# Performance work log

Hardware: AMD Instinct MI355X
Metric: run time of the kernel (lower is better)

Reference implementation:

```python
import jax, jax.numpy as jnp
import numpy as np

B, S, D = 2, 2048, 1024
H, HD = 16, 64          # n_heads, head_dim
FF, HID = 4096, 8192    # d_ff, swiglu hidden (= 2*d_ff)


def _ln(x, eps=1e-5):
    # non-parametric LayerNorm (fp8_layernorm_noparam in source)
    m = jnp.mean(x, axis=-1, keepdims=True)
    v = jnp.var(x, axis=-1, keepdims=True)
    return (x - m) * jax.lax.rsqrt(v + eps)


def setup_inputs() -> dict:
    key = jax.random.key(0)
    ks = jax.random.split(key, 7)
    s = 0.02  # init std
    return {
        "x": jax.random.normal(ks[0], (B, S, D), jnp.float32),
        "Wq": jax.random.normal(ks[1], (D, D), jnp.float32) * s,
        "Wk": jax.random.normal(ks[2], (D, D), jnp.float32) * s,
        "Wv": jax.random.normal(ks[3], (D, D), jnp.float32) * s,
        "Wo": jax.random.normal(ks[4], (D, D), jnp.float32) * s,
        "Wff": jax.random.normal(ks[5], (HID, D), jnp.float32) * s,
        "Wout": jax.random.normal(ks[6], (FF, D), jnp.float32).T * s,  # [D, FF] -> stored as Linear weight [D_out=D, D_in=FF]
    }


def reference(x, Wq, Wk, Wv, Wo, Wff, Wout):
    b, s, d = x.shape
    # attention sub-block
    h = _ln(x)
    q = (h @ Wq.T).reshape(b, s, H, HD).transpose(0, 2, 1, 3)  # [B,H,S,HD]
    k = (h @ Wk.T).reshape(b, s, H, HD).transpose(0, 2, 1, 3)
    v = (h @ Wv.T).reshape(b, s, H, HD).transpose(0, 2, 1, 3)
    scale = 1.0 / float(HD) ** 0.5
    scores = jnp.einsum('bhqd,bhkd->bhqk', q, k) * scale        # [B,H,S,S] naive full matrix
    causal = jnp.tril(jnp.ones((s, s), dtype=bool))
    scores = jnp.where(causal, scores, jnp.finfo(scores.dtype).min)
    attn = jax.nn.softmax(scores, axis=-1)
    att = jnp.einsum('bhqk,bhkd->bhqd', attn, v)                # [B,H,S,HD]
    att = att.transpose(0, 2, 1, 3).reshape(b, s, d)
    x = x + att @ Wo.T
    # MLP sub-block (SwiGLU, OLMo Llama-style)
    h2 = _ln(x)
    ff = h2 @ Wff.T                                             # [B,S,HID]
    x1, x2 = jnp.split(ff, 2, axis=-1)
    g = jax.nn.silu(x1) * x2                                    # [B,S,FF]
    return x + g @ Wout.T
```

## Files before the change

### kernel.cpp

```cpp
#include <hip/hip_runtime.h>
#include <hip/hip_bf16.h>

#define B_ 2
#define S_ 2048
#define D_ 1024
#define H_ 16
#define FF_ 4096
#define M_ (B_*S_)

using u16 = unsigned short;
using u32 = unsigned int;
typedef __attribute__((ext_vector_type(8))) short short8;
typedef __attribute__((ext_vector_type(4))) float f32x4;
typedef __attribute__((ext_vector_type(16))) float f32x16;
typedef __attribute__((ext_vector_type(4))) unsigned short u16x4;
typedef __attribute__((ext_vector_type(4))) unsigned int u32x4;

static __device__ __forceinline__ u16 f2bf(float f) {
  __hip_bfloat16 h = __float2bfloat16(f);
  return *reinterpret_cast<u16*>(&h);
}
static __device__ __forceinline__ float bf2f(u16 u) {
  __hip_bfloat16 h; *reinterpret_cast<u16*>(&h) = u;
  return __bfloat162float(h);
}

#define GLDS(gp, lp) __builtin_amdgcn_global_load_lds( \
    (const __attribute__((address_space(1))) void*)(gp), \
    (__attribute__((address_space(3))) void*)(lp), 16, 0, 0)

#define MFMA16(a, b, c) __builtin_amdgcn_mfma_f32_16x16x32_bf16(a, b, c, 0, 0, 0)
#define VMC(n) asm volatile("s_waitcnt vmcnt(" #n ")" ::: "memory")
#define BAR() __builtin_amdgcn_s_barrier()

__global__ __launch_bounds__(256) void conv_f32_bf16(
    const float* __restrict__ src, u16* __restrict__ dst, int n4) {
  int i = blockIdx.x * 256 + threadIdx.x;
  if (i < n4) {
    float4 v = reinterpret_cast<const float4*>(src)[i];
    u16x4 o;
    o.x = f2bf(v.x); o.y = f2bf(v.y); o.z = f2bf(v.z); o.w = f2bf(v.w);
    reinterpret_cast<u16x4*>(dst)[i] = o;
  }
}

__global__ __launch_bounds__(256) void ln_rows(
    const float* __restrict__ x, u16* __restrict__ out) {
  int row = blockIdx.x;
  int t = threadIdx.x;
  float4 v = reinterpret_cast<const float4*>(x + (size_t)row * D_)[t];
  float s  = v.x + v.y + v.z + v.w;
  float ss = v.x*v.x + v.y*v.y + v.z*v.z + v.w*v.w;
  #pragma unroll
  for (int off = 1; off < 64; off <<= 1) {
    s  += __shfl_xor(s,  off, 64);
    ss += __shfl_xor(ss, off, 64);
  }
  __shared__ float rs[4], rss[4];
  int wid = t >> 6;
  if ((t & 63) == 0) { rs[wid] = s; rss[wid] = ss; }
  __syncthreads();
  s  = rs[0] + rs[1] + rs[2] + rs[3];
  ss = rss[0] + rss[1] + rss[2] + rss[3];
  float mean = s * (1.0f / D_);
  float var  = ss * (1.0f / D_) - mean * mean;
  float r = rsqrtf(var + 1e-5f);
  u16x4 o;
  o.x = f2bf((v.x - mean) * r);
  o.y = f2bf((v.y - mean) * r);
  o.z = f2bf((v.z - mean) * r);
  o.w = f2bf((v.w - mean) * r);
  reinterpret_cast<u16x4*>(out + (size_t)row * D_)[t] = o;
}

template<int MODE>
__global__ __launch_bounds__(256, 2) void gemm_bt2(
    const u16* __restrict__ A, const u16* __restrict__ W,
    void* __restrict__ C, const u16* __restrict__ aux,
    const float* __restrict__ res, int M, int N, int K)
{
  __shared__ u16 lds[32768];
  const int tid = threadIdx.x;
  const int wid = tid >> 6, lane = tid & 63;
  const int g = lane >> 4, c = lane & 15;
  const int gridN = N >> 7;
  int nwg = gridDim.x;
  int lin = blockIdx.x;
  lin = (lin & 7) * (nwg >> 3) + (lin >> 3);
  const int bm = lin / gridN, bn = lin % gridN;
  const int wm = wid >> 1, wn = wid & 1;
  const int NT = K >> 6;

  f32x4 acc[4][4];
  #pragma unroll
  for (int i = 0; i < 4; i++)
    #pragma unroll
    for (int j = 0; j < 4; j++) acc[i][j] = {0.f, 0.f, 0.f, 0.f};

  auto stage = [&](int sel, int t) {
    const u16* src = sel ? W : A;
    const int tilerow = (sel ? bn : bm) * 128;
    char* dst = (char*)&lds[sel * 16384 + (t & 1) * 8192];
    #pragma unroll
    for (int i = 0; i < 4; i++) {
      int j = i * 256 + tid;
      int row = j >> 3, col16 = j & 7;
      const u16* gp = src + (size_t)(tilerow + row) * K + t * 64 + ((col16 ^ (row & 7)) << 3);
      GLDS(gp, dst + j * 16);
    }
  };

  stage(0, 0); stage(1, 0);
  __syncthreads();

  for (int t = 0; t < NT; t++) {
    const int buf = t & 1;
    if (t + 1 < NT) { stage(0, t + 1); stage(1, t + 1); }

    short8 af[2][4], bfr[2][4];
    #pragma unroll
    for (int ks = 0; ks < 2; ks++)
      #pragma unroll
      for (int m = 0; m < 4; m++) {
        int rh = wm * 64 + m * 16 + c;
        af[ks][m] = *reinterpret_cast<const short8*>(
            &lds[buf * 8192 + rh * 64 + ((((ks << 2) | g) ^ (rh & 7)) << 3)]);
      }
    #pragma unroll
    for (int ks = 0; ks < 2; ks++)
      #pragma unroll
      for (int n = 0; n < 4; n++) {
        int rh = wn * 64 + n * 16 + c;
        bfr[ks][n] = *reinterpret_cast<const short8*>(
            &lds[16384 + buf * 8192 + rh * 64 + ((((ks << 2) | g) ^ (rh & 7)) << 3)]);
      }
    __builtin_amdgcn_s_setprio(1);
    #pragma unroll
    for (int m = 0; m < 4; m++)
      #pragma unroll
      for (int n = 0; n < 4; n++) {
        acc[m][n] = MFMA16(af[0][m], bfr[0][n], acc[m][n]);
        acc[m][n] = MFMA16(af[1][m], bfr[1][n], acc[m][n]);
      }
    __builtin_amdgcn_s_setprio(0);
    __syncthreads();
  }

  #pragma unroll
  for (int m = 0; m < 4; m++)
    #pragma unroll
    for (int n = 0; n < 4; n++)
      #pragma unroll
      for (int r = 0; r < 4; r++) {
        int gr = bm * 128 + wm * 64 + m * 16 + g * 4 + r;
        int gc = bn * 128 + wn * 64 + n * 16 + c;
        size_t idx = (size_t)gr * N + gc;
        float v = acc[m][n][r];
        if (MODE == 0) {
          ((u16*)C)[idx] = f2bf(v);
        } else if (MODE == 1) {
          ((float*)C)[idx] = v + res[idx];
        } else if (MODE == 2) {
          ((u16*)C)[idx] = f2bf(v / (1.0f + __expf(-v)));
        } else {
          ((u16*)C)[idx] = f2bf(v * bf2f(aux[idx]));
        }
      }
}

__global__ __launch_bounds__(256) void transpose_v(
    const u16* __restrict__ qkv, u16* __restrict__ vT) {
  __shared__ u16 t[64][66];
  int bh = blockIdx.y;
  int s0 = blockIdx.x * 64;
  int b = bh >> 4, h = bh & 15;
  int tid = threadIdx.x;
  #pragma unroll
  for (int it = 0; it < 2; it++) {
    int idx = it * 256 + tid;
    int row = idx >> 3;
    int cc  = (idx & 7) * 8;
    const u16* src = qkv + ((size_t)(b * S_ + s0 + row)) * 3072 + 2048 + h * 64 + cc;
    short8 v = *reinterpret_cast<const short8*>(src);
    #pragma unroll
    for (int j = 0; j < 8; j++) t[row][cc + j] = (u16)v[j];
  }
  __syncthreads();
  #pragma unroll
  for (int it = 0; it < 2; it++) {
    int idx = it * 256 + tid;
    int d  = idx >> 3;
    int sc = (idx & 7) * 8;
    short8 o;
    #pragma unroll
    for (int j = 0; j < 8; j++) o[j] = (short)t[sc + j][d];
    *reinterpret_cast<short8*>(vT + ((size_t)bh * 64 + d) * S_ + s0 + sc) = o;
  }
}

__global__ __launch_bounds__(256) void attn_split(
    const u16* __restrict__ qkv, const u16* __restrict__ vT,
    u16* __restrict__ pO, float* __restrict__ pML) {
  __shared__ u16 Kl[2][2048];
  __shared__ u16 Vl[2][2048];
  const int tid  = threadIdx.x;
  const int lane = tid & 63;
  const int wid  = tid >> 6;
  const int l31  = lane & 31;
  const int half = lane >> 5;

  int lin = blockIdx.x;
  int swz = (lin & 7) * 160 + (lin >> 3);
  int bh  = swz / 40;
  int j   = swz - bh * 40;
  int qq = 15, rem = j;
  while (rem > (qq >> 2)) { rem -= (qq >> 2) + 1; qq--; }
  int ci = rem;
  const int qt  = qq * 4 + wid;
  const int kt0 = ci * 16;
  const int nt  = min(qq * 4 + 3, kt0 + 15) - kt0;
  int ubase = (qt < 16) ? qt : (qt < 32) ? 16 + (qt - 16) * 2 + ci
            : (qt < 48) ? 48 + (qt - 32) * 3 + ci : 96 + (qt - 48) * 4 + ci;
  const int punit = bh * 160 + ubase;

  const int b = bh >> 4, hd = bh & 15;
  const int q_base = qt * 32;

  const u16* Qb = qkv + ((size_t)(b * S_ + q_base + l31)) * 3072 + hd * 64;
  const u16* Kb = qkv + (size_t)b * S_ * 3072 + 1024 + hd * 64;
  const u16* Vt = vT + (size_t)bh * 64 * S_;

  short8 qf[4];
  #pragma unroll
  for (int dt = 0; dt < 4; dt++) {
    short8 v = *reinterpret_cast<const short8*>(Qb + dt * 16 + half * 8);
    #pragma unroll
    for (int jj = 0; jj < 8; jj++) v[jj] = (short)f2bf(bf2f((u16)v[jj]) * 0.125f);
    qf[dt] = v;
  }

  auto stageKV = [&](int kt, int buf) {
    {
      int row = tid >> 3, cs = tid & 7;
      int c = cs ^ (row & 7);
      const u16* gp = Kb + (size_t)(kt * 32 + row) * 3072 + c * 8;
      GLDS(gp, (char*)&Kl[buf][0] + tid * 16);
    }
    {
      int row = tid >> 2, cs = tid & 3;
      int c = cs ^ (row & 3);
      const u16* gp = Vt + (size_t)row * S_ + kt * 32 + c * 8;
      GLDS(gp, (char*)&Vl[buf][0] + tid * 16);
    }
  };

  f32x16 o0, o1;
  #pragma unroll
  for (int r = 0; r < 16; r++) { o0[r] = 0.f; o1[r] = 0.f; }
  float m = -1e30f, lsum = 0.f;

  stageKV(kt0, 0);
  VMC(0); BAR();

  for (int i = 0; ; i++) {
    const int kt = kt0 + i;
    const int buf = i & 1;
    if (i < nt) stageKV(kt + 1, buf ^ 1);

    if (kt <= qt) {
      const bool diag = (kt == qt);
      short8 kfr[4], vfr[4];
      #pragma unroll
      for (int dt = 0; dt < 4; dt++) {
        int cs = (dt * 2 + half) ^ (l31 & 7);
        kfr[dt] = *reinterpret_cast<const short8*>((const char*)&Kl[buf][0] + l31 * 128 + cs * 16);
      }
      {
        int r0 = l31, r1 = 32 + l31;
        vfr[0] = *reinterpret_cast<const short8*>((const char*)&Vl[buf][0] + r0 * 64 + ((half       ^ (r0 & 3)) * 16));
        vfr[1] = *reinterpret_cast<const short8*>((const char*)&Vl[buf][0] + r0 * 64 + (((2 + half) ^ (r0 & 3)) * 16));
        vfr[2] = *reinterpret_cast<const short8*>((const char*)&Vl[buf][0] + r1 * 64 + ((half       ^ (r1 & 3)) * 16));
        vfr[3] = *reinterpret_cast<const short8*>((const char*)&Vl[buf][0] + r1 * 64 + (((2 + half) ^ (r1 & 3)) * 16));
      }

      f32x16 s;
      #pragma unroll
      for (int r = 0; r < 16; r++) s[r] = 0.f;
      __builtin_amdgcn_s_setprio(1);
      #pragma unroll
      for (int dt = 0; dt < 4; dt++)
        s = __builtin_amdgcn_mfma_f32_32x32x16_bf16(kfr[dt], qf[dt], s, 0, 0, 0);
      __builtin_amdgcn_s_setprio(0);

      float p[16];
      #pragma unroll
      for (int r = 0; r < 16; r++) {
        p[r] = s[r];
        if (diag) {
          int kloc = half * 4 + (r & 3) + 8 * (r >> 2);
          if (kloc > l31) p[r] = -1e30f;
        }
      }
      float rm = p[0];
      #pragma unroll
      for (int r = 1; r < 16; r++) rm = fmaxf(rm, p[r]);
      rm = fmaxf(rm, __shfl_xor(rm, 32, 64));

      if (__any(rm > m + 8.0f)) {
        float mn = fmaxf(m, rm);
        float alpha = __expf(m - mn);
        m = mn;
        lsum *= alpha;
        #pragma unroll
        for (int r = 0; r < 16; r++) {
          int row = (r & 3) + 8 * (r >> 2) + 4 * half;
          float ar = __shfl(alpha, row, 64);
          o0[r] *= ar; o1[r] *= ar;
        }
      }
      float rs = 0.f;
      #pragma unroll
      for (int r = 0; r < 16; r++) { p[r] = __expf(p[r] - m); rs += p[r]; }
      rs += __shfl_xor(rs, 32, 64);
      lsum += rs;

      u32 pk[8], sp[8];
      #pragma unroll
      for (int ii = 0; ii < 8; ii++) {
        pk[ii] = (u32)f2bf(p[2 * ii]) | ((u32)f2bf(p[2 * ii + 1]) << 16);
        sp[ii] = (u32)__shfl_xor((int)pk[ii], 32, 64);
      }
      u32x4 a0 = { half ? sp[2] : pk[0], half ? sp[3] : pk[1],
                   half ? pk[2] : sp[0], half ? pk[3] : sp[1] };
      u32x4 a1 = { half ? sp[6] : pk[4], half ? sp[7] : pk[5],
                   half ? pk[6] : sp[4], half ? pk[7] : sp[5] };
      short8 pa0 = *reinterpret_cast<short8*>(&a0);
      short8 pa1 = *reinterpret_cast<short8*>(&a1);

      __builtin_amdgcn_s_setprio(1);
      o0 = __builtin_amdgcn_mfma_f32_32x32x16_bf16(pa0, vfr[0], o0, 0, 0, 0);
      o0 = __builtin_amdgcn_mfma_f32_32x32x16_bf16(pa1, vfr[1], o0, 0, 0, 0);
      o1 = __builtin_amdgcn_mfma_f32_32x32x16_bf16(pa0, vfr[2], o1, 0, 0, 0);
      o1 = __builtin_amdgcn_mfma_f32_32x32x16_bf16(pa1, vfr[3], o1, 0, 0, 0);
      __builtin_amdgcn_s_setprio(0);
    }

    if (i == nt) break;
    VMC(0); BAR();
  }

  #pragma unroll
  for (int r = 0; r < 16; r++) {
    int row = (r & 3) + 8 * (r >> 2) + 4 * half;
    pO[(size_t)punit * 2048 + row * 64 + l31]      = f2bf(o0[r]);
    pO[(size_t)punit * 2048 + row * 64 + 32 + l31] = f2bf(o1[r]);
  }
  if (half == 0) {
    pML[punit * 64 + l31]      = m;
    pML[punit * 64 + 32 + l31] = lsum;
  }
}

__global__ __launch_bounds__(256) void attn_combine(
    const u16* __restrict__ pO, const float* __restrict__ pML,
    u16* __restrict__ att) {
  int gw = blockIdx.x;
  int bh = gw >> 6, qt = gw & 63;
  int b = bh >> 4, hd = bh & 15;
  int nc = (qt >> 4) + 1;
  int base = (qt < 16) ? qt : (qt < 32) ? 16 + (qt - 16) * 2
           : (qt < 48) ? 48 + (qt - 32) * 3 : 96 + (qt - 48) * 4;
  int p0 = bh * 160 + base;
  int q  = threadIdx.x >> 3;
  int d  = (threadIdx.x & 7) * 8;

  float m0 = pML[p0 * 64 + q];
  float l0 = pML[p0 * 64 + 32 + q];
  float m1 = nc > 1 ? pML[(p0 + 1) * 64 + q]      : -1e30f;
  float l1 = nc > 1 ? pML[(p0 + 1) * 64 + 32 + q] : 0.f;
  float m2 = nc > 2 ? pML[(p0 + 2) * 64 + q]      : -1e30f;
  float l2 = nc > 2 ? pML[(p0 + 2) * 64 + 32 + q] : 0.f;
  float m3 = nc > 3 ? pML[(p0 + 3) * 64 + q]      : -1e30f;
  float l3 = nc > 3 ? pML[(p0 + 3) * 64 + 32 + q] : 0.f;
  float M = fmaxf(fmaxf(m0, m1), fmaxf(m2, m3));
  float w0 = __expf(m0 - M), w1 = __expf(m1 - M);
  float w2 = __expf(m2 - M), w3 = __expf(m3 - M);
  float L = l0 * w0 + l1 * w1 + l2 * w2 + l3 * w3;
  float invL = 1.0f / L;

  float o[8];
  short8 v0 = *reinterpret_cast<const short8*>(&pO[(size_t)p0 * 2048 + q * 64 + d]);
  #pragma unroll
  for (int jj = 0; jj < 8; jj++) o[jj] = bf2f((u16)v0[jj]) * w0;
  if (nc > 1) {
    short8 v = *reinterpret_cast<const short8*>(&pO[(size_t)(p0 + 1) * 2048 + q * 64 + d]);
    #pragma unroll
    for (int jj = 0; jj < 8; jj++) o[jj] += bf2f((u16)v[jj]) * w1;
  }
  if (nc > 2) {
    short8 v = *reinterpret_cast<const short8*>(&pO[(size_t)(p0 + 2) * 2048 + q * 64 + d]);
    #pragma unroll
    for (int jj = 0; jj < 8; jj++) o[jj] += bf2f((u16)v[jj]) * w2;
  }
  if (nc > 3) {
    short8 v = *reinterpret_cast<const short8*>(&pO[(size_t)(p0 + 3) * 2048 + q * 64 + d]);
    #pragma unroll
    for (int jj = 0; jj < 8; jj++) o[jj] += bf2f((u16)v[jj]) * w3;
  }
  short8 ov;
  #pragma unroll
  for (int jj = 0; jj < 8; jj++) ov[jj] = (short)f2bf(o[jj] * invL);
  *reinterpret_cast<short8*>(
      &att[((size_t)(b * S_ + qt * 32 + q)) * D_ + hd * 64 + d]) = ov;
}

extern "C" void kernel_launch(void* const* d_in, const int* in_sizes, int n_in,
                              void* d_out, int out_size, void* d_ws, size_t ws_size,
                              hipStream_t stream) {
  (void)in_sizes; (void)n_in; (void)out_size; (void)ws_size;
  const float* x    = (const float*)d_in[0];
  const float* Wq   = (const float*)d_in[1];
  const float* Wk   = (const float*)d_in[2];
  const float* Wv   = (const float*)d_in[3];
  const float* Wo   = (const float*)d_in[4];
  const float* Wff  = (const float*)d_in[5];
  const float* Wout = (const float*)d_in[6];
  float* out = (float*)d_out;

  char* ws = (char*)d_ws;
  u16*   wqkv = (u16*)(ws);
  u16*   wo   = (u16*)(ws + 6291456);
  u16*   wff  = (u16*)(ws + 8388608);
  u16*   wout = (u16*)(ws + 25165824);
  float* x1   = (float*)(ws + 33554432);
  char*  P    = ws + 50331648;
  u16*   hbuf = (u16*)(P);
  u16*   qkv  = (u16*)(P + 8388608);
  u16*   vT   = (u16*)(P + 33554432);
  u16*   att  = (u16*)(P + 41943040);
  u16*   pO   = (u16*)(P + 50331648);
  float* pML  = (float*)(P + 71303168);
  u16*   h2   = (u16*)(P);
  u16*   s1   = (u16*)(P + 8388608);
  u16*   gbuf = (u16*)(P + 41943040);

  conv_f32_bf16<<<1024, 256, 0, stream>>>(Wq, wqkv,               262144);
  conv_f32_bf16<<<1024, 256, 0, stream>>>(Wk, wqkv + 1048576,     262144);
  conv_f32_bf16<<<1024, 256, 0, stream>>>(Wv, wqkv + 2097152,     262144);
  conv_f32_bf16<<<1024, 256, 0, stream>>>(Wo, wo,                 262144);
  conv_f32_bf16<<<8192, 256, 0, stream>>>(Wff, wff,               2097152);
  conv_f32_bf16<<<4096, 256, 0, stream>>>(Wout, wout,             1048576);

  ln_rows<<<M_, 256, 0, stream>>>(x, hbuf);
  gemm_bt2<0><<<dim3(768), 256, 0, stream>>>(hbuf, wqkv, qkv, nullptr, nullptr, M_, 3072, 1024);
  transpose_v<<<dim3(32, 32), 256, 0, stream>>>(qkv, vT);
  attn_split<<<dim3(1280), 256, 0, stream>>>(qkv, vT, pO, pML);
  attn_combine<<<dim3(2048), 256, 0, stream>>>(pO, pML, att);
  gemm_bt2<1><<<dim3(256), 256, 0, stream>>>(att, wo, x1, nullptr, x, M_, 1024, 1024);

  ln_rows<<<M_, 256, 0, stream>>>(x1, h2);
  gemm_bt2<2><<<dim3(1024), 256, 0, stream>>>(h2, wff, s1, nullptr, nullptr, M_, 4096, 1024);
  gemm_bt2<3><<<dim3(1024), 256, 0, stream>>>(h2, wff + 4194304, gbuf, s1, nullptr, M_, 4096, 1024);
  gemm_bt2<1><<<dim3(256), 256, 0, stream>>>(gbuf, wout, out, nullptr, x1, M_, 1024, 4096);
}
```

Before: 277.9 us.

## Fuse SwiGLU gate and up GEMMs into one kernel; use exp2 softmax

After: 281.8 us. Within noise of the previous version (+1.4%).

```diff
diff --git a/kernel.cpp b/kernel.cpp
--- a/kernel.cpp
+++ b/kernel.cpp
@@ -160,11 +160,92 @@
           ((u16*)C)[idx] = f2bf(v);
         } else if (MODE == 1) {
           ((float*)C)[idx] = v + res[idx];
-        } else if (MODE == 2) {
-          ((u16*)C)[idx] = f2bf(v / (1.0f + __expf(-v)));
-        } else {
-          ((u16*)C)[idx] = f2bf(v * bf2f(aux[idx]));
         }
+      }
+}
+
+__global__ __launch_bounds__(256, 2) void gemm_ff(
+    const u16* __restrict__ A, const u16* __restrict__ W,
+    u16* __restrict__ Cout, int M, int N, int K)
+{
+  __shared__ u16 lds[24576];
+  const int tid = threadIdx.x;
+  const int wid = tid >> 6, lane = tid & 63;
+  const int g = lane >> 4, c = lane & 15;
+  const int gridN = N >> 7;
+  int nwg = gridDim.x;
+  int lin = blockIdx.x;
+  lin = (lin & 7) * (nwg >> 3) + (lin >> 3);
+  const int bm = lin / gridN, bn = lin % gridN;
+  const int wm = wid >> 1, wn = wid & 1;
+  const int NT = K >> 5;
+
+  f32x4 ac1[4][4], ac2[4][4];
+  #pragma unroll
+  for (int i = 0; i < 4; i++)
+    #pragma unroll
+    for (int j = 0; j < 4; j++) { ac1[i][j] = {0.f,0.f,0.f,0.f}; ac2[i][j] = {0.f,0.f,0.f,0.f}; }
+
+  auto stage = [&](int sel, int t) {
+    const u16* src = (sel == 0) ? A : W;
+    const int rowbase = (sel == 0) ? bm * 128 : (sel == 1 ? bn * 128 : 4096 + bn * 128);
+    char* dst = (char*)&lds[sel * 8192 + (t & 1) * 4096];
+    #pragma unroll
+    for (int i = 0; i < 2; i++) {
+      int j = i * 256 + tid;
+      int r = j >> 2, cslot = j & 3;
+      int csrc = cslot ^ ((r >> 1) & 3);
+      const u16* gp = src + (size_t)(rowbase + r) * K + t * 32 + csrc * 8;
+      GLDS(gp, dst + j * 16);
+    }
+  };
+
+  stage(0, 0); stage(1, 0); stage(2, 0);
+  __syncthreads();
+
+  for (int t = 0; t < NT; t++) {
+    const int buf = t & 1;
+    if (t + 1 < NT) { stage(0, t + 1); stage(1, t + 1); stage(2, t + 1); }
+
+    short8 af[4], b1f[4], b2f[4];
+    #pragma unroll
+    for (int m = 0; m < 4; m++) {
+      int rh = wm * 64 + m * 16 + c;
+      af[m] = *reinterpret_cast<const short8*>(
+          &lds[buf * 4096 + rh * 32 + ((g ^ ((rh >> 1) & 3)) << 3)]);
+    }
+    #pragma unroll
+    for (int n = 0; n < 4; n++) {
+      int rh = wn * 64 + n * 16 + c;
+      b1f[n] = *reinterpret_cast<const short8*>(
+          &lds[8192 + buf * 4096 + rh * 32 + ((g ^ ((rh >> 1) & 3)) << 3)]);
+      b2f[n] = *reinterpret_cast<const short8*>(
+          &lds[16384 + buf * 4096 + rh * 32 + ((g ^ ((rh >> 1) & 3)) << 3)]);
+    }
+    __builtin_amdgcn_s_setprio(1);
+    #pragma unroll
+    for (int m = 0; m < 4; m++)
+      #pragma unroll
+      for (int n = 0; n < 4; n++) {
+        ac1[m][n] = MFMA16(af[m], b1f[n], ac1[m][n]);
+        ac2[m][n] = MFMA16(af[m], b2f[n], ac2[m][n]);
+      }
+    __builtin_amdgcn_s_setprio(0);
+    __syncthreads();
+  }
+
+  #pragma unroll
+  for (int m = 0; m < 4; m++)
+    #pragma unroll
+    for (int n = 0; n < 4; n++)
+      #pragma unroll
+      for (int r = 0; r < 4; r++) {
+        int gr = bm * 128 + wm * 64 + m * 16 + g * 4 + r;
+        int gc = bn * 128 + wn * 64 + n * 16 + c;
+        float v1 = ac1[m][n][r];
+        float v2 = ac2[m][n][r];
+        float gv = (v1 / (1.0f + __expf(-v1))) * v2;
+        Cout[(size_t)gr * N + gc] = f2bf(gv);
       }
 }
 
@@ -235,7 +316,7 @@
   for (int dt = 0; dt < 4; dt++) {
     short8 v = *reinterpret_cast<const short8*>(Qb + dt * 16 + half * 8);
     #pragma unroll
-    for (int jj = 0; jj < 8; jj++) v[jj] = (short)f2bf(bf2f((u16)v[jj]) * 0.125f);
+    for (int jj = 0; jj < 8; jj++) v[jj] = (short)f2bf(bf2f((u16)v[jj]) * 0.18033688f);
     qf[dt] = v;
   }
 
@@ -301,14 +382,17 @@
           if (kloc > l31) p[r] = -1e30f;
         }
       }
-      float rm = p[0];
-      #pragma unroll
-      for (int r = 1; r < 16; r++) rm = fmaxf(rm, p[r]);
+      float t8[8];
+      #pragma unroll
+      for (int r = 0; r < 8; r++) t8[r] = fmaxf(p[r], p[r + 8]);
+      float t4a = fmaxf(t8[0], t8[4]), t4b = fmaxf(t8[1], t8[5]);
+      float t4c = fmaxf(t8[2], t8[6]), t4d = fmaxf(t8[3], t8[7]);
+      float rm = fmaxf(fmaxf(t4a, t4b), fmaxf(t4c, t4d));
       rm = fmaxf(rm, __shfl_xor(rm, 32, 64));
 
-      if (__any(rm > m + 8.0f)) {
+      if (__any(rm > m + 11.0f)) {
         float mn = fmaxf(m, rm);
-        float alpha = __expf(m - mn);
+        float alpha = exp2f(m - mn);
         m = mn;
         lsum *= alpha;
         #pragma unroll
@@ -320,7 +404,7 @@
       }
       float rs = 0.f;
       #pragma unroll
-      for (int r = 0; r < 16; r++) { p[r] = __expf(p[r] - m); rs += p[r]; }
+      for (int r = 0; r < 16; r++) { p[r] = exp2f(p[r] - m); rs += p[r]; }
       rs += __shfl_xor(rs, 32, 64);
       lsum += rs;
 
@@ -383,8 +467,8 @@
   float m3 = nc > 3 ? pML[(p0 + 3) * 64 + q]      : -1e30f;
   float l3 = nc > 3 ? pML[(p0 + 3) * 64 + 32 + q] : 0.f;
   float M = fmaxf(fmaxf(m0, m1), fmaxf(m2, m3));
-  float w0 = __expf(m0 - M), w1 = __expf(m1 - M);
-  float w2 = __expf(m2 - M), w3 = __expf(m3 - M);
+  float w0 = exp2f(m0 - M), w1 = exp2f(m1 - M);
+  float w2 = exp2f(m2 - M), w3 = exp2f(m3 - M);
   float L = l0 * w0 + l1 * w1 + l2 * w2 + l3 * w3;
   float invL = 1.0f / L;
 
@@ -441,7 +525,6 @@
   u16*   pO   = (u16*)(P + 50331648);
   float* pML  = (float*)(P + 71303168);
   u16*   h2   = (u16*)(P);
-  u16*   s1   = (u16*)(P + 8388608);
   u16*   gbuf = (u16*)(P + 41943040);
 
   conv_f32_bf16<<<1024, 256, 0, stream>>>(Wq, wqkv,               262144);
@@ -459,7 +542,6 @@
   gemm_bt2<1><<<dim3(256), 256, 0, stream>>>(att, wo, x1, nullptr, x, M_, 1024, 1024);
 
   ln_rows<<<M_, 256, 0, stream>>>(x1, h2);
-  gemm_bt2<2><<<dim3(1024), 256, 0, stream>>>(h2, wff, s1, nullptr, nullptr, M_, 4096, 1024);
-  gemm_bt2<3><<<dim3(1024), 256, 0, stream>>>(h2, wff + 4194304, gbuf, s1, nullptr, M_, 4096, 1024);
+  gemm_ff<<<dim3(1024), 256, 0, stream>>>(h2, wff, gbuf, M_, 4096, 1024);
   gemm_bt2<1><<<dim3(256), 256, 0, stream>>>(gbuf, wout, out, nullptr, x1, M_, 1024, 4096);
 }
```
